# Kernel optimization log

Hardware: AMD Instinct MI355X
Metric: run time of the kernel (lower is better)

## Reference

```python
import jax, jax.numpy as jnp
import numpy as np

EMBED_DIM = 4096
NUM_HEADS = 64
RANK = 1
B, T = 64, 64  # T must equal NUM_HEADS for the mask broadcast (faithful to source)


def setup_inputs() -> dict:
    key = jax.random.key(0)
    k1, k2, k3, k4, k5 = jax.random.split(key, 5)
    C = EMBED_DIM
    s = 0.02
    return {
        "x": jax.random.normal(k1, (B, T, C), dtype=jnp.float32),
        "W_atten": jax.random.normal(k2, (3 * C, C), dtype=jnp.float32) * s,
        "b_atten": jax.random.normal(k3, (3 * C,), dtype=jnp.float32) * s,
        "W_proj": jax.random.normal(k4, (C, C), dtype=jnp.float32) * s,
        "b_proj": jax.random.normal(k5, (C,), dtype=jnp.float32) * s,
    }


def reference(x, W_atten, b_atten, W_proj, b_proj):
    Bx, Tx, C = x.shape
    H = NUM_HEADS
    hd = C // H
    r = RANK
    qkv = jnp.einsum("btc,oc->bto", x, W_atten) + b_atten  # (B,T,3C)
    q, k, v = jnp.split(qkv, 3, axis=2)
    # view (B,T,rank,H,hd) then transpose(1,2) -> (B,rank,T,H,hd)
    def reshp(t):
        return t.reshape(Bx, Tx, r, H, hd).transpose(0, 2, 1, 3, 4)
    q, k, v = reshp(q), reshp(k), reshp(v)
    scale = (1.0 / np.sqrt(hd)) * (r ** 0.5)
    # attention across heads at each timestep: (B,rank,T,H,H)
    att = jnp.einsum("brtqd,brtkd->brtqk", q, k) * scale
    # tril[:T,:T] broadcasts onto trailing (H,H) dims (requires T == H)
    tril = jnp.tril(jnp.ones((Tx, Tx), dtype=jnp.float32))
    att = jnp.where(tril == 0, -jnp.inf, att)
    att = jax.nn.softmax(att, axis=-1)
    y = jnp.einsum("brtqk,brtkd->brtqd", att, v)  # (B,rank,T,H,hd)
    y = y.transpose(0, 2, 1, 3, 4).reshape(Bx, Tx, C)
    return jnp.einsum("btc,oc->bto", y, W_proj) + b_proj
```

## Files before the change

### kernel.cpp

```cpp
#include <hip/hip_runtime.h>
#include <stdint.h>

#define M_TOK   4096
#define C_DIM   4096
#define N_QKV   12288
#define KD      4096
#define NT2     32

typedef __bf16 bf16x8 __attribute__((ext_vector_type(8)));
typedef float  f32x4  __attribute__((ext_vector_type(4)));
typedef unsigned short ushort8 __attribute__((ext_vector_type(8)));

__device__ __forceinline__ unsigned short f2bf(float f) {
  unsigned int u = __builtin_bit_cast(unsigned int, f);
  u = (u + 0x7FFFu + ((u >> 16) & 1u)) >> 16;
  return (unsigned short)u;
}

__global__ __launch_bounds__(256) void cvt_f32_bf16(const float* __restrict__ in,
                                                    unsigned short* __restrict__ out,
                                                    int n16) {
  int idx = blockIdx.x * 256 + threadIdx.x;
  if (idx >= n16) return;
  const float4* p = (const float4*)in;
  float4 a = p[idx * 2], b = p[idx * 2 + 1];
  uint4 r;
  r.x = (unsigned)f2bf(a.x) | ((unsigned)f2bf(a.y) << 16);
  r.y = (unsigned)f2bf(a.z) | ((unsigned)f2bf(a.w) << 16);
  r.z = (unsigned)f2bf(b.x) | ((unsigned)f2bf(b.y) << 16);
  r.w = (unsigned)f2bf(b.z) | ((unsigned)f2bf(b.w) << 16);
  ((uint4*)out)[idx] = r;
}

#define GLLDS(gp, lp) \
  __builtin_amdgcn_global_load_lds((const __attribute__((address_space(1))) unsigned int*)(gp), \
                                   (__attribute__((address_space(3))) unsigned int*)(lp), 16, 0, 0)


#define STAGE_A(buf, hf, tau) do {                                         \
    const unsigned short* g_ = Ag + (size_t)((hf) * 64) * KD + (tau) * 64; \
    unsigned short* d_ = As + (buf) * 16384 + (hf) * 8192 + t * 8;         \
    GLLDS(g_, d_);                                                         \
    GLLDS(g_ + (size_t)128 * KD, d_ + 4096);                               \
  } while (0)

#define STAGE_B(buf, nhf, tau) do {                                         \
    const unsigned short* g_ = Bg + (size_t)((nhf) * 32) * KD + (tau) * 64; \
    unsigned short* d_ = Bs + (buf) * 16384 + (nhf) * 8192 + t * 8;         \
    GLLDS(g_, d_);                                                          \
    GLLDS(g_ + (size_t)128 * KD, d_ + 4096);                                \
  } while (0)

#define LDA_(buf, mh) do {                                                        \
    const unsigned short* pa_ = As + (buf) * 16384 + (mh) * 8192 + wm * 4096 + lr * 64; \
    afk[0][0] = *(const bf16x8*)(pa_ + 0 * 1024 + ck0);                           \
    afk[0][1] = *(const bf16x8*)(pa_ + 1 * 1024 + ck0);                           \
    afk[0][2] = *(const bf16x8*)(pa_ + 2 * 1024 + ck0);                           \
    afk[0][3] = *(const bf16x8*)(pa_ + 3 * 1024 + ck0);                           \
    afk[1][0] = *(const bf16x8*)(pa_ + 0 * 1024 + ck1);                           \
    afk[1][1] = *(const bf16x8*)(pa_ + 1 * 1024 + ck1);                           \
    afk[1][2] = *(const bf16x8*)(pa_ + 2 * 1024 + ck1);                           \
    afk[1][3] = *(const bf16x8*)(pa_ + 3 * 1024 + ck1);                           \
  } while (0)

#define LDB_(buf, nhf, dst) do {                                                  \
    const unsigned short* pb_ = Bs + (buf) * 16384 + (nhf) * 8192 + wn * 2048 + lr * 64; \
    dst[0][0] = *(const bf16x8*)(pb_ + 0 * 1024 + ck0);                           \
    dst[0][1] = *(const bf16x8*)(pb_ + 1 * 1024 + ck0);                           \
    dst[1][0] = *(const bf16x8*)(pb_ + 0 * 1024 + ck1);                           \
    dst[1][1] = *(const bf16x8*)(pb_ + 1 * 1024 + ck1);                           \
  } while (0)

#define LDAB_(buf, mh, nhf, dst) do {                                             \
    const unsigned short* pa_ = As + (buf) * 16384 + (mh) * 8192 + wm * 4096 + lr * 64; \
    const unsigned short* pb_ = Bs + (buf) * 16384 + (nhf) * 8192 + wn * 2048 + lr * 64; \
    afk[0][0] = *(const bf16x8*)(pa_ + 0 * 1024 + ck0);                           \
    afk[0][1] = *(const bf16x8*)(pa_ + 1 * 1024 + ck0);                           \
    afk[0][2] = *(const bf16x8*)(pa_ + 2 * 1024 + ck0);                           \
    afk[0][3] = *(const bf16x8*)(pa_ + 3 * 1024 + ck0);                           \
    dst[0][0] = *(const bf16x8*)(pb_ + 0 * 1024 + ck0);                           \
    dst[0][1] = *(const bf16x8*)(pb_ + 1 * 1024 + ck0);                           \
    afk[1][0] = *(const bf16x8*)(pa_ + 0 * 1024 + ck1);                           \
    afk[1][1] = *(const bf16x8*)(pa_ + 1 * 1024 + ck1);                           \
    afk[1][2] = *(const bf16x8*)(pa_ + 2 * 1024 + ck1);                           \
    afk[1][3] = *(const bf16x8*)(pa_ + 3 * 1024 + ck1);                           \
    dst[1][0] = *(const bf16x8*)(pb_ + 0 * 1024 + ck1);                           \
    dst[1][1] = *(const bf16x8*)(pb_ + 1 * 1024 + ck1);                           \
  } while (0)

#define QUAD_(mh, nhf, bsrc) do {                                                 \
    __builtin_amdgcn_s_setprio(1);                                                \
    _Pragma("unroll") for (int kk_ = 0; kk_ < 2; ++kk_)                           \
    _Pragma("unroll") for (int mt_ = 0; mt_ < 4; ++mt_)                           \
    _Pragma("unroll") for (int nt_ = 0; nt_ < 2; ++nt_)                           \
      acc[mh][nhf][mt_][nt_] = __builtin_amdgcn_mfma_f32_16x16x32_bf16(           \
          afk[kk_][mt_], bsrc[kk_][nt_], acc[mh][nhf][mt_][nt_], 0, 0, 0);        \
    __builtin_amdgcn_s_setprio(0);                                                \
  } while (0)

#define BAR_() do {                                        \
    asm volatile("" ::: "memory");                         \
    __builtin_amdgcn_s_barrier();                          \
    asm volatile("" ::: "memory");                         \
  } while (0)

#define VM6_() asm volatile("s_waitcnt vmcnt(6)" ::: "memory")

template <int OUT_BF16>
__global__ __launch_bounds__(512, 2) void gemm256(const unsigned short* __restrict__ A,
                                                  const unsigned short* __restrict__ B,
                                                  const float* __restrict__ bias,
                                                  void* __restrict__ Cptr,
                                                  int N) {
  __shared__ __align__(16) unsigned short As[32768];
  __shared__ __align__(16) unsigned short Bs[32768];

  const int t   = threadIdx.x;
  const int nwg = gridDim.x;
  const int bid = blockIdx.x;
  const int wg  = (bid & 7) * (nwg >> 3) + (bid >> 3);
  const int bm  = wg & 15;
  const int bn  = wg >> 4;

  const int w  = t >> 6, l = t & 63;
  const int wm = w >> 2, wn = w & 3;
  const int lr = l & 15, lq = l >> 4;
  const int ck0 = (lq ^ (lr & 7)) * 8;
  const int ck1 = ck0 ^ 32;

  const int r8  = t >> 3;
  const int kcs = ((t & 7) ^ (r8 & 7)) * 8;
  const unsigned short* Ag = A + (size_t)(bm * 256 + r8) * KD + kcs;
  const unsigned short* Bg = B + (size_t)(bn * 256 + ((t >> 8) << 6) + (r8 & 31)) * KD + kcs;

  f32x4 acc[2][2][4][2] = {};
  bf16x8 afk[2][4], bA[2][2], bB[2][2];

  STAGE_A(0, 0, 0); STAGE_B(0, 0, 0); STAGE_B(0, 1, 0); STAGE_A(0, 1, 0);
  STAGE_A(1, 0, 1); STAGE_B(1, 0, 1); STAGE_B(1, 1, 1);
  VM6_();
  BAR_();

#pragma unroll 1
  for (int i = 0; i < NT2; ++i) {
    const int t1 = 2 * i + 1;
    const int t2 = (2 * i + 2 < 64) ? 2 * i + 2 : 63;
    const int t3 = (2 * i + 3 < 64) ? 2 * i + 3 : 63;
    STAGE_A(1, 1, t1);
    LDAB_(0, 0, 0, bA);
    QUAD_(0, 0, bA);
    BAR_();
    STAGE_A(0, 0, t2);
    LDB_(0, 1, bB);
    QUAD_(0, 1, bB);
    BAR_();
    STAGE_B(0, 0, t2);
    LDA_(0, 1);
    QUAD_(1, 0, bA);
    BAR_();
    STAGE_B(0, 1, t2);
    QUAD_(1, 1, bB);
    VM6_();
    BAR_();
    STAGE_A(0, 1, t2);
    LDAB_(1, 0, 0, bA);
    QUAD_(0, 0, bA);
    BAR_();
    STAGE_A(1, 0, t3);
    LDB_(1, 1, bB);
    QUAD_(0, 1, bB);
    BAR_();
    STAGE_B(1, 0, t3);
    LDA_(1, 1);
    QUAD_(1, 0, bA);
    BAR_();
    STAGE_B(1, 1, t3);
    QUAD_(1, 1, bB);
    VM6_();
    BAR_();
  }

  asm volatile("s_waitcnt vmcnt(0)" ::: "memory");

  const int row0 = bm * 256 + wm * 128 + lq * 4;
  const int col0 = bn * 256 + wn * 64 + lr;
#pragma unroll
  for (int nhf = 0; nhf < 2; ++nhf)
#pragma unroll
    for (int nt = 0; nt < 2; ++nt) {
      const int col = col0 + nhf * 32 + nt * 16;
      const float bv = bias[col];
#pragma unroll
      for (int mh = 0; mh < 2; ++mh)
#pragma unroll
        for (int mt = 0; mt < 4; ++mt) {
          const int row = row0 + mh * 64 + mt * 16;
#pragma unroll
          for (int rg = 0; rg < 4; ++rg) {
            float v = acc[mh][nhf][mt][nt][rg] + bv;
            if (OUT_BF16)
              ((unsigned short*)Cptr)[(size_t)(row + rg) * N + col] = f2bf(v);
            else
              ((float*)Cptr)[(size_t)(row + rg) * N + col] = v;
          }
        }
    }
}

#define AST 72

__global__ __launch_bounds__(64) void attn_mfma(const unsigned short* __restrict__ qkv,
                                                unsigned short* __restrict__ y) {
  __shared__ __align__(16) unsigned short Ks[64 * AST];
  __shared__ __align__(16) unsigned short Vs[64 * AST];
  const int l  = threadIdx.x;
  const int lr = l & 15;
  const int lq = l >> 4;
  const size_t base = (size_t)blockIdx.x * 12288;

  {
    const int jr = l >> 3;
    const int cc = (l & 7) * 8;
#pragma unroll
    for (int c = 0; c < 8; ++c) {
      const int j = c * 8 + jr;
      *(uint4*)(Ks + j * AST + cc) = *(const uint4*)(qkv + base + 4096 + (size_t)j * 64 + cc);
      *(uint4*)(Vs + j * AST + cc) = *(const uint4*)(qkv + base + 8192 + (size_t)j * 64 + cc);
    }
  }

  bf16x8 aq[4][2];
#pragma unroll
  for (int it = 0; it < 4; ++it)
#pragma unroll
    for (int kk = 0; kk < 2; ++kk)
      aq[it][kk] = *(const bf16x8*)(qkv + base + (size_t)(it * 16 + lr) * 64 + kk * 32 + lq * 8);

  __syncthreads();

  f32x4 acc[4][4] = {};
#pragma unroll
  for (int kk = 0; kk < 2; ++kk) {
    bf16x8 bk[4];
#pragma unroll
    for (int jt = 0; jt < 4; ++jt)
      bk[jt] = *(const bf16x8*)(Ks + (jt * 16 + lr) * AST + kk * 32 + lq * 8);
#pragma unroll
    for (int it = 0; it < 4; ++it)
#pragma unroll
      for (int jt = 0; jt < 4; ++jt)
        acc[it][jt] = __builtin_amdgcn_mfma_f32_16x16x32_bf16(aq[it][kk], bk[jt], acc[it][jt], 0, 0, 0);
  }

#pragma unroll
  for (int it = 0; it < 4; ++it) {
#pragma unroll
    for (int rg = 0; rg < 4; ++rg) {
      const int row = it * 16 + lq * 4 + rg;
      float mx = -1e30f;
#pragma unroll
      for (int jt = 0; jt < 4; ++jt) {
        const int col = jt * 16 + lr;
        float s = acc[it][jt][rg] * 0.125f;
        s = (col <= row) ? s : -1e30f;
        acc[it][jt][rg] = s;
        mx = fmaxf(mx, s);
      }
#pragma unroll
      for (int d = 1; d < 16; d <<= 1)
        mx = fmaxf(mx, __shfl_xor(mx, d));
      float sum = 0.f;
#pragma unroll
      for (int jt = 0; jt < 4; ++jt) {
        float e = __expf(acc[it][jt][rg] - mx);
        acc[it][jt][rg] = e;
        sum += e;
      }
#pragma unroll
      for (int d = 1; d < 16; d <<= 1)
        sum += __shfl_xor(sum, d);
      const float inv = 1.f / sum;
#pragma unroll
      for (int jt = 0; jt < 4; ++jt)
        acc[it][jt][rg] *= inv;
    }
  }

#pragma unroll
  for (int it = 0; it < 4; ++it)
#pragma unroll
    for (int rg = 0; rg < 4; ++rg) {
      const int row = it * 16 + lq * 4 + rg;
#pragma unroll
      for (int jt = 0; jt < 4; ++jt)
        Ks[row * AST + jt * 16 + lr] = f2bf(acc[it][jt][rg]);
    }
  __syncthreads();

  f32x4 out[4][4] = {};
#pragma unroll
  for (int kk = 0; kk < 2; ++kk) {
    bf16x8 ap[4];
#pragma unroll
    for (int it = 0; it < 4; ++it)
      ap[it] = *(const bf16x8*)(Ks + (it * 16 + lr) * AST + kk * 32 + lq * 8);
#pragma unroll
    for (int dt = 0; dt < 4; ++dt) {
      ushort8 vt;
#pragma unroll
      for (int jj = 0; jj < 8; ++jj)
        vt[jj] = Vs[(kk * 32 + lq * 8 + jj) * AST + dt * 16 + lr];
      const bf16x8 bv = __builtin_bit_cast(bf16x8, vt);
#pragma unroll
      for (int it = 0; it < 4; ++it)
        out[it][dt] = __builtin_amdgcn_mfma_f32_16x16x32_bf16(ap[it], bv, out[it][dt], 0, 0, 0);
    }
  }

  unsigned short* yrow = y + (size_t)blockIdx.x * 4096;
#pragma unroll
  for (int it = 0; it < 4; ++it)
#pragma unroll
    for (int rg = 0; rg < 4; ++rg) {
      const int i = it * 16 + lq * 4 + rg;
#pragma unroll
      for (int dt = 0; dt < 4; ++dt)
        yrow[i * 64 + dt * 16 + lr] = f2bf(out[it][dt][rg]);
    }
}

extern "C" void kernel_launch(void* const* d_in, const int* in_sizes, int n_in,
                              void* d_out, int out_size, void* d_ws, size_t ws_size,
                              hipStream_t stream) {
  const float* x  = (const float*)d_in[0];
  const float* Wa = (const float*)d_in[1];
  const float* ba = (const float*)d_in[2];
  const float* Wp = (const float*)d_in[3];
  const float* bp = (const float*)d_in[4];
  float* out = (float*)d_out;

  unsigned short* regA = (unsigned short*)d_ws;
  unsigned short* regB = regA + (size_t)16777216;
  unsigned short* regC = regB + (size_t)50331648;
  unsigned short* xb   = regA;
  unsigned short* Wab  = regB;
  unsigned short* qkvb = regC;
  unsigned short* Wpb  = regA;
  unsigned short* yb   = regB;

  cvt_f32_bf16<<<(16777216 / 8) / 256, 256, 0, stream>>>(x, xb, 16777216 / 8);
  cvt_f32_bf16<<<(50331648 / 8) / 256, 256, 0, stream>>>(Wa, Wab, 50331648 / 8);

  gemm256<1><<<dim3((M_TOK / 256) * (N_QKV / 256)), dim3(512), 0, stream>>>(
      xb, Wab, ba, (void*)qkvb, N_QKV);

  cvt_f32_bf16<<<(16777216 / 8) / 256, 256, 0, stream>>>(Wp, Wpb, 16777216 / 8);

  attn_mfma<<<M_TOK, 64, 0, stream>>>(qkvb, yb);

  gemm256<0><<<dim3((M_TOK / 256) * (C_DIM / 256)), dim3(512), 0, stream>>>(
      yb, Wpb, bp, (void*)out, C_DIM);
}
```

Baseline: 950.9 us.

## Simplify GEMM pipeline to plain double buffering with full vmcnt waits

Replaces the interleaved 8-phase staging schedule, which kept several global-to-LDS loads in flight across barriers using vmcnt(6), with a simple two-stage double buffer. Each half-iteration now issues all loads for the next tile, computes the current one, then waits on vmcnt(0) and synchronizes once. This cuts the barrier count per iteration from 8 to 2 and makes the schedule easier to reason about. The cost is less overlap, since every memory wait drains all outstanding loads.

```diff
diff --git a/kernel.cpp b/kernel.cpp
--- a/kernel.cpp
+++ b/kernel.cpp
@@ -104,7 +104,7 @@
     asm volatile("" ::: "memory");                         \
   } while (0)
 
-#define VM6_() asm volatile("s_waitcnt vmcnt(6)" ::: "memory")
+#define VM0_() asm volatile("s_waitcnt vmcnt(0)" ::: "memory")
 
 template <int OUT_BF16>
 __global__ __launch_bounds__(512, 2) void gemm256(const unsigned short* __restrict__ A,
@@ -136,51 +136,31 @@
   f32x4 acc[2][2][4][2] = {};
   bf16x8 afk[2][4], bA[2][2], bB[2][2];
 
-  STAGE_A(0, 0, 0); STAGE_B(0, 0, 0); STAGE_B(0, 1, 0); STAGE_A(0, 1, 0);
-  STAGE_A(1, 0, 1); STAGE_B(1, 0, 1); STAGE_B(1, 1, 1);
-  VM6_();
+  STAGE_A(0, 0, 0); STAGE_A(0, 1, 0); STAGE_B(0, 0, 0); STAGE_B(0, 1, 0);
+  VM0_();
   BAR_();
 
 #pragma unroll 1
   for (int i = 0; i < NT2; ++i) {
     const int t1 = 2 * i + 1;
     const int t2 = (2 * i + 2 < 64) ? 2 * i + 2 : 63;
-    const int t3 = (2 * i + 3 < 64) ? 2 * i + 3 : 63;
-    STAGE_A(1, 1, t1);
-    LDAB_(0, 0, 0, bA);
-    QUAD_(0, 0, bA);
+
+    STAGE_A(1, 0, t1); STAGE_A(1, 1, t1); STAGE_B(1, 0, t1); STAGE_B(1, 1, t1);
+    LDAB_(0, 0, 0, bA); QUAD_(0, 0, bA);
+    LDB_(0, 1, bB);     QUAD_(0, 1, bB);
+    LDA_(0, 1);         QUAD_(1, 0, bA);
+                        QUAD_(1, 1, bB);
+    VM0_();
     BAR_();
-    STAGE_A(0, 0, t2);
-    LDB_(0, 1, bB);
-    QUAD_(0, 1, bB);
+
+    STAGE_A(0, 0, t2); STAGE_A(0, 1, t2); STAGE_B(0, 0, t2); STAGE_B(0, 1, t2);
+    LDAB_(1, 0, 0, bA); QUAD_(0, 0, bA);
+    LDB_(1, 1, bB);     QUAD_(0, 1, bB);
+    LDA_(1, 1);         QUAD_(1, 0, bA);
+                        QUAD_(1, 1, bB);
+    VM0_();
     BAR_();
-    STAGE_B(0, 0, t2);
-    LDA_(0, 1);
-    QUAD_(1, 0, bA);
-    BAR_();
-    STAGE_B(0, 1, t2);
-    QUAD_(1, 1, bB);
-    VM6_();
-    BAR_();
-    STAGE_A(0, 1, t2);
-    LDAB_(1, 0, 0, bA);
-    QUAD_(0, 0, bA);
-    BAR_();
-    STAGE_A(1, 0, t3);
-    LDB_(1, 1, bB);
-    QUAD_(0, 1, bB);
-    BAR_();
-    STAGE_B(1, 0, t3);
-    LDA_(1, 1);
-    QUAD_(1, 0, bA);
-    BAR_();
-    STAGE_B(1, 1, t3);
-    QUAD_(1, 1, bB);
-    VM6_();
-    BAR_();
-  }
-
-  asm volatile("s_waitcnt vmcnt(0)" ::: "memory");
+  }
 
   const int row0 = bm * 256 + wm * 128 + lq * 4;
   const int col0 = bn * 256 + wn * 64 + lr;
```

Result: no change. 944.5 us (-0.7%).

## Double-buffer A fragments in registers and pin LDS/MFMA schedule with sched barriers

Applied to the files above, without the earlier changes.

Splits the A-fragment registers into two banks so the fragments for both M halves can be loaded ahead of use, and reorders the four MFMA quads per K-tile to reuse them. It issues LDS reads before the global-to-LDS staging, adds explicit lgkmcnt waits and sched_barrier fences so the compiler cannot interleave the phases, and doubles the number of workgroup barriers per stage. The aim is to hide LDS read latency behind MFMA work. The cost is higher register pressure and more barrier synchronisation per iteration.

```diff
diff --git a/kernel.cpp b/kernel.cpp
--- a/kernel.cpp
+++ b/kernel.cpp
@@ -51,16 +51,16 @@
     GLLDS(g_ + (size_t)128 * KD, d_ + 4096);                                \
   } while (0)
 
-#define LDA_(buf, mh) do {                                                        \
+#define LDA2_(buf, mh, bank) do {                                                 \
     const unsigned short* pa_ = As + (buf) * 16384 + (mh) * 8192 + wm * 4096 + lr * 64; \
-    afk[0][0] = *(const bf16x8*)(pa_ + 0 * 1024 + ck0);                           \
-    afk[0][1] = *(const bf16x8*)(pa_ + 1 * 1024 + ck0);                           \
-    afk[0][2] = *(const bf16x8*)(pa_ + 2 * 1024 + ck0);                           \
-    afk[0][3] = *(const bf16x8*)(pa_ + 3 * 1024 + ck0);                           \
-    afk[1][0] = *(const bf16x8*)(pa_ + 0 * 1024 + ck1);                           \
-    afk[1][1] = *(const bf16x8*)(pa_ + 1 * 1024 + ck1);                           \
-    afk[1][2] = *(const bf16x8*)(pa_ + 2 * 1024 + ck1);                           \
-    afk[1][3] = *(const bf16x8*)(pa_ + 3 * 1024 + ck1);                           \
+    bank[0][0] = *(const bf16x8*)(pa_ + 0 * 1024 + ck0);                          \
+    bank[0][1] = *(const bf16x8*)(pa_ + 1 * 1024 + ck0);                          \
+    bank[0][2] = *(const bf16x8*)(pa_ + 2 * 1024 + ck0);                          \
+    bank[0][3] = *(const bf16x8*)(pa_ + 3 * 1024 + ck0);                          \
+    bank[1][0] = *(const bf16x8*)(pa_ + 0 * 1024 + ck1);                          \
+    bank[1][1] = *(const bf16x8*)(pa_ + 1 * 1024 + ck1);                          \
+    bank[1][2] = *(const bf16x8*)(pa_ + 2 * 1024 + ck1);                          \
+    bank[1][3] = *(const bf16x8*)(pa_ + 3 * 1024 + ck1);                          \
   } while (0)
 
 #define LDB_(buf, nhf, dst) do {                                                  \
@@ -71,40 +71,22 @@
     dst[1][1] = *(const bf16x8*)(pb_ + 1 * 1024 + ck1);                           \
   } while (0)
 
-#define LDAB_(buf, mh, nhf, dst) do {                                             \
-    const unsigned short* pa_ = As + (buf) * 16384 + (mh) * 8192 + wm * 4096 + lr * 64; \
-    const unsigned short* pb_ = Bs + (buf) * 16384 + (nhf) * 8192 + wn * 2048 + lr * 64; \
-    afk[0][0] = *(const bf16x8*)(pa_ + 0 * 1024 + ck0);                           \
-    afk[0][1] = *(const bf16x8*)(pa_ + 1 * 1024 + ck0);                           \
-    afk[0][2] = *(const bf16x8*)(pa_ + 2 * 1024 + ck0);                           \
-    afk[0][3] = *(const bf16x8*)(pa_ + 3 * 1024 + ck0);                           \
-    dst[0][0] = *(const bf16x8*)(pb_ + 0 * 1024 + ck0);                           \
-    dst[0][1] = *(const bf16x8*)(pb_ + 1 * 1024 + ck0);                           \
-    afk[1][0] = *(const bf16x8*)(pa_ + 0 * 1024 + ck1);                           \
-    afk[1][1] = *(const bf16x8*)(pa_ + 1 * 1024 + ck1);                           \
-    afk[1][2] = *(const bf16x8*)(pa_ + 2 * 1024 + ck1);                           \
-    afk[1][3] = *(const bf16x8*)(pa_ + 3 * 1024 + ck1);                           \
-    dst[1][0] = *(const bf16x8*)(pb_ + 0 * 1024 + ck1);                           \
-    dst[1][1] = *(const bf16x8*)(pb_ + 1 * 1024 + ck1);                           \
-  } while (0)
-
-#define QUAD_(mh, nhf, bsrc) do {                                                 \
+#define QUAD_(mh, nhf, abank, bsrc) do {                                          \
     __builtin_amdgcn_s_setprio(1);                                                \
     _Pragma("unroll") for (int kk_ = 0; kk_ < 2; ++kk_)                           \
     _Pragma("unroll") for (int mt_ = 0; mt_ < 4; ++mt_)                           \
     _Pragma("unroll") for (int nt_ = 0; nt_ < 2; ++nt_)                           \
       acc[mh][nhf][mt_][nt_] = __builtin_amdgcn_mfma_f32_16x16x32_bf16(           \
-          afk[kk_][mt_], bsrc[kk_][nt_], acc[mh][nhf][mt_][nt_], 0, 0, 0);        \
+          abank[kk_][mt_], bsrc[kk_][nt_], acc[mh][nhf][mt_][nt_], 0, 0, 0);      \
     __builtin_amdgcn_s_setprio(0);                                                \
   } while (0)
 
-#define BAR_() do {                                        \
-    asm volatile("" ::: "memory");                         \
-    __builtin_amdgcn_s_barrier();                          \
-    asm volatile("" ::: "memory");                         \
-  } while (0)
-
-#define VM6_() asm volatile("s_waitcnt vmcnt(6)" ::: "memory")
+#define SB_()  __builtin_amdgcn_sched_barrier(0)
+#define BAR_() do { asm volatile("" ::: "memory");  __builtin_amdgcn_s_barrier(); \
+                    asm volatile("" ::: "memory"); } while (0)
+#define LGKM0_() do { asm volatile("s_waitcnt lgkmcnt(0)" ::: "memory"); SB_(); } while (0)
+#define LGKM8_() do { asm volatile("s_waitcnt lgkmcnt(8)" ::: "memory"); SB_(); } while (0)
+#define VM6_()   asm volatile("s_waitcnt vmcnt(6)" ::: "memory")
 
 template <int OUT_BF16>
 __global__ __launch_bounds__(512, 2) void gemm256(const unsigned short* __restrict__ A,
@@ -134,7 +116,7 @@
   const unsigned short* Bg = B + (size_t)(bn * 256 + ((t >> 8) << 6) + (r8 & 31)) * KD + kcs;
 
   f32x4 acc[2][2][4][2] = {};
-  bf16x8 afk[2][4], bA[2][2], bB[2][2];
+  bf16x8 afk0[2][4], afk1[2][4], bA[2][2], bB[2][2];
 
   STAGE_A(0, 0, 0); STAGE_B(0, 0, 0); STAGE_B(0, 1, 0); STAGE_A(0, 1, 0);
   STAGE_A(1, 0, 1); STAGE_B(1, 0, 1); STAGE_B(1, 1, 1);
@@ -146,36 +128,74 @@
     const int t1 = 2 * i + 1;
     const int t2 = (2 * i + 2 < 64) ? 2 * i + 2 : 63;
     const int t3 = (2 * i + 3 < 64) ? 2 * i + 3 : 63;
+
+    SB_();
+    LDA2_(0, 0, afk0);
+    LDB_(0, 0, bA);
+    SB_();
     STAGE_A(1, 1, t1);
-    LDAB_(0, 0, 0, bA);
-    QUAD_(0, 0, bA);
-    BAR_();
+    BAR_();
+    LGKM0_();
+    QUAD_(0, 0, afk0, bA);
+    SB_();
+    BAR_();
+    SB_();
+    LDB_(0, 1, bB);
+    SB_();
+    LDA2_(0, 1, afk1);
+    SB_();
     STAGE_A(0, 0, t2);
-    LDB_(0, 1, bB);
-    QUAD_(0, 1, bB);
+    BAR_();
+    LGKM8_();
+    QUAD_(0, 1, afk0, bB);
+    SB_();
     BAR_();
     STAGE_B(0, 0, t2);
-    LDA_(0, 1);
-    QUAD_(1, 0, bA);
+    BAR_();
+    LGKM0_();
+    QUAD_(1, 1, afk1, bB);
+    SB_();
     BAR_();
     STAGE_B(0, 1, t2);
-    QUAD_(1, 1, bB);
+    BAR_();
+    SB_();
+    QUAD_(1, 0, afk1, bA);
+    SB_();
     VM6_();
     BAR_();
+
+    SB_();
+    LDA2_(1, 0, afk0);
+    LDB_(1, 0, bA);
+    SB_();
     STAGE_A(0, 1, t2);
-    LDAB_(1, 0, 0, bA);
-    QUAD_(0, 0, bA);
-    BAR_();
+    BAR_();
+    LGKM0_();
+    QUAD_(0, 0, afk0, bA);
+    SB_();
+    BAR_();
+    SB_();
+    LDB_(1, 1, bB);
+    SB_();
+    LDA2_(1, 1, afk1);
+    SB_();
     STAGE_A(1, 0, t3);
-    LDB_(1, 1, bB);
-    QUAD_(0, 1, bB);
+    BAR_();
+    LGKM8_();
+    QUAD_(0, 1, afk0, bB);
+    SB_();
     BAR_();
     STAGE_B(1, 0, t3);
-    LDA_(1, 1);
-    QUAD_(1, 0, bA);
+    BAR_();
+    LGKM0_();
+    QUAD_(1, 1, afk1, bB);
+    SB_();
     BAR_();
     STAGE_B(1, 1, t3);
-    QUAD_(1, 1, bB);
+    BAR_();
+    SB_();
+    QUAD_(1, 0, afk1, bA);
+    SB_();
     VM6_();
     BAR_();
   }
```

Result: faster. 884.6 us (-7.0%).
